# Kernel tuning notes

Hardware: AMD Instinct MI355X
Metric: run time of the kernel (lower is better)

Reference implementation:

```python
import jax, jax.numpy as jnp
import numpy as np

B, S, D, H = 2, 2048, 1024, 16
HEAD_DIM = D // H
WINDOW = 256
DILATION = 1
NEG = jnp.float32(-1e9)


def _build_attn_mask(seq_len):
    # Faithful port of torch _build_attn_mask for causal=True, stencil kind='local'.
    idx = jnp.arange(seq_len)
    diff = idx[None, :] - idx[:, None]  # diff[i, j] = j - i (torch diff is idx.unsqueeze(0)-idx.unsqueeze(1))
    # causal: -inf strictly above diagonal (j > i)
    mask = jnp.where(diff > 0, -jnp.inf, 0.0).astype(jnp.float32)
    # stencil allow: |diff| <= window and |diff| % dilation == 0
    cond = (jnp.abs(diff) <= WINDOW) & (jnp.abs(diff) % DILATION == 0)
    allowed = jnp.where(cond, 0.0, -jnp.inf).astype(jnp.float32)
    # torch.maximum: allow() can UNMASK causally-masked positions inside the window
    mask = jnp.maximum(mask, allowed)
    # clamp(min=-1e9)
    return jnp.maximum(mask, NEG)


def setup_inputs() -> dict:
    key = jax.random.key(0)
    k = jax.random.split(key, 5)
    return {
        "x": jax.random.normal(k[0], (B, S, D), dtype=jnp.float32),
        "in_proj_w": jax.random.normal(k[1], (3 * D, D), dtype=jnp.float32) * (D ** -0.5),
        "in_proj_b": jax.random.normal(k[2], (3 * D,), dtype=jnp.float32) * 0.02,
        "out_proj_w": jax.random.normal(k[3], (D, D), dtype=jnp.float32) * (D ** -0.5),
        "out_proj_b": jax.random.normal(k[4], (D,), dtype=jnp.float32) * 0.02,
    }


def reference(x, in_proj_w, in_proj_b, out_proj_w, out_proj_b):
    b, s, d = x.shape
    # fused qkv projection (torch nn.MultiheadAttention in_proj)
    qkv = x @ in_proj_w.T + in_proj_b  # [b, s, 3d]
    q, k, v = jnp.split(qkv, 3, axis=-1)

    def to_heads(t):
        return t.reshape(b, s, H, HEAD_DIM).transpose(0, 2, 1, 3)  # [b, h, s, hd]

    q, k, v = to_heads(q), to_heads(k), to_heads(v)
    scale = jnp.float32(HEAD_DIM) ** -0.5
    scores = jnp.einsum("bhqd,bhkd->bhqk", q * scale, k)  # [b, h, s, s]
    mask = _build_attn_mask(s)  # [s, s]
    scores = scores + mask[None, None, :, :]
    attn = jax.nn.softmax(scores, axis=-1)
    out = jnp.einsum("bhqk,bhkd->bhqd", attn, v)  # [b, h, s, hd]
    out = out.transpose(0, 2, 1, 3).reshape(b, s, d)
    return out @ out_proj_w.T + out_proj_b
```

## Files before the change

kernel.cpp:

```cpp
#include <hip/hip_runtime.h>
#include <cstddef>

#define BATCH   2
#define SEQ     2048
#define DMODEL  1024
#define NH      16
#define HDIM    64
#define WIN     256
#define MTOT    4096

typedef __bf16 bf16;
typedef __attribute__((ext_vector_type(8)))  __bf16 bf16x8;
typedef __attribute__((ext_vector_type(4)))  float  f32x4;
typedef __attribute__((ext_vector_type(16))) float  f32x16;

#define GLOAD_LDS(gp, lp) __builtin_amdgcn_global_load_lds( \
    (const __attribute__((address_space(1))) void*)(gp),    \
    (__attribute__((address_space(3))) void*)(lp), 16, 0, 0)

__device__ __forceinline__ float fast_exp2(float x) {
#if __has_builtin(__builtin_amdgcn_exp2f)
  return __builtin_amdgcn_exp2f(x);
#else
  float r; asm("v_exp_f32 %0, %1" : "=v"(r) : "v"(x)); return r;
#endif
}

__global__ __launch_bounds__(256)
void cvt_all(const float* __restrict__ x, const float* __restrict__ w1,
             const float* __restrict__ w2, bf16* __restrict__ xh,
             bf16* __restrict__ xl, bf16* __restrict__ w1h,
             bf16* __restrict__ w1l, bf16* __restrict__ w2h,
             bf16* __restrict__ w2l) {
  const int bid = blockIdx.x;
  const float* s; bf16 *hp, *lp; int base;
  if (bid < 2048)      { s = x;  hp = xh;  lp = xl;  base = bid * 2048; }
  else if (bid < 3584) { s = w1; hp = w1h; lp = w1l; base = (bid - 2048) * 2048; }
  else                 { s = w2; hp = w2h; lp = w2l; base = (bid - 3584) * 2048; }
  const int i = base + threadIdx.x * 8;
  float4 a = *(const float4*)(s + i);
  float4 c = *(const float4*)(s + i + 4);
  const float f[8] = {a.x, a.y, a.z, a.w, c.x, c.y, c.z, c.w};
  bf16x8 vh, vl;
#pragma unroll
  for (int j = 0; j < 8; ++j) {
    bf16 hh = (bf16)f[j];
    vh[j] = hh;
    vl[j] = (bf16)(f[j] - (float)hh);
  }
  *(bf16x8*)(hp + i) = vh;
  *(bf16x8*)(lp + i) = vl;
}

__global__ __launch_bounds__(256, 4)
void gemm_qkv_fused(const bf16* __restrict__ xh, const bf16* __restrict__ xl,
                    const bf16* __restrict__ w1h, const bf16* __restrict__ w1l,
                    const float* __restrict__ b1,
                    bf16* __restrict__ Qh, bf16* __restrict__ Ql,
                    bf16* __restrict__ Kt, bf16* __restrict__ Vt) {
  __shared__ bf16 sAh[128 * 32];
  __shared__ bf16 sAl[128 * 32];
  __shared__ bf16 sBh[128 * 32];
  __shared__ bf16 sBl[64 * 32];

  const int t = threadIdx.x, w = t >> 6, lane = t & 63;
  const int ln15 = lane & 15, quad = lane >> 4;
  const int drow = lane >> 2;
  const int dkcol = (lane & 3) * 8;
  const int bid = blockIdx.x;

  if (bid < 512) {
    const int bm = (bid >> 4) * 128;
    const int bn = (bid & 15) * 64;

    f32x4 acc[2][4];
#pragma unroll
    for (int i = 0; i < 2; ++i)
#pragma unroll
      for (int j = 0; j < 4; ++j)
#pragma unroll
        for (int r = 0; r < 4; ++r) acc[i][j][r] = 0.f;

    for (int k0 = 0; k0 < DMODEL; k0 += 32) {
      __syncthreads();
#pragma unroll
      for (int half = 0; half < 2; ++half) {
        const int r = w * 32 + half * 16 + drow;
        const size_t goffA = (size_t)(bm + r) * DMODEL + k0 + dkcol;
        const int loff = (w * 32 + half * 16) * 32;
        GLOAD_LDS(xh + goffA, sAh + loff);
        GLOAD_LDS(xl + goffA, sAl + loff);
      }
      {
        const int r = w * 16 + drow;
        const size_t goffB = (size_t)(bn + r) * DMODEL + k0 + dkcol;
        const int loff = (w * 16) * 32;
        GLOAD_LDS(w1h + goffB, sBh + loff);
        GLOAD_LDS(w1l + goffB, sBl + loff);
      }
      __syncthreads();

      bf16x8 afh[2], afl[2], bfh[4], bfl[4];
#pragma unroll
      for (int mt = 0; mt < 2; ++mt) {
        const int off = (w * 32 + mt * 16 + ln15) * 32 + quad * 8;
        afh[mt] = *(const bf16x8*)&sAh[off];
        afl[mt] = *(const bf16x8*)&sAl[off];
      }
#pragma unroll
      for (int nt = 0; nt < 4; ++nt) {
        const int off = (nt * 16 + ln15) * 32 + quad * 8;
        bfh[nt] = *(const bf16x8*)&sBh[off];
        bfl[nt] = *(const bf16x8*)&sBl[off];
      }
#pragma unroll
      for (int mt = 0; mt < 2; ++mt)
#pragma unroll
        for (int nt = 0; nt < 4; ++nt) {
          acc[mt][nt] = __builtin_amdgcn_mfma_f32_16x16x32_bf16(afh[mt], bfh[nt], acc[mt][nt], 0, 0, 0);
          acc[mt][nt] = __builtin_amdgcn_mfma_f32_16x16x32_bf16(afh[mt], bfl[nt], acc[mt][nt], 0, 0, 0);
          acc[mt][nt] = __builtin_amdgcn_mfma_f32_16x16x32_bf16(afl[mt], bfh[nt], acc[mt][nt], 0, 0, 0);
        }
    }

    float bbcol[4];
#pragma unroll
    for (int nt = 0; nt < 4; ++nt) bbcol[nt] = b1[bn + nt * 16 + ln15];

#pragma unroll
    for (int mt = 0; mt < 2; ++mt)
#pragma unroll
      for (int r = 0; r < 4; ++r) {
        const size_t grow = (size_t)(bm + w * 32 + mt * 16 + quad * 4 + r);
#pragma unroll
        for (int nt = 0; nt < 4; ++nt) {
          const int col = bn + nt * 16 + ln15;
          const float v = acc[mt][nt][r] + bbcol[nt];
          const bf16 hh = (bf16)v;
          Qh[grow * 1024 + col] = hh;
          Ql[grow * 1024 + col] = (bf16)(v - (float)hh);
        }
      }
  } else if (bid < 768) {
    const int kid = bid - 512;
    const int bm = (kid >> 3) * 128, bn = 1024 + (kid & 7) * 128;
    const int wrow = (w & 1) * 64, wcol = (w >> 1) * 64;

    f32x4 acc[4][4];
#pragma unroll
    for (int i = 0; i < 4; ++i)
#pragma unroll
      for (int j = 0; j < 4; ++j)
#pragma unroll
        for (int r = 0; r < 4; ++r) acc[i][j][r] = 0.f;

    for (int k0 = 0; k0 < DMODEL; k0 += 32) {
      __syncthreads();
#pragma unroll
      for (int half = 0; half < 2; ++half) {
        const int r = w * 32 + half * 16 + drow;
        const int loff = (w * 32 + half * 16) * 32;
        GLOAD_LDS(xh + (size_t)(bm + r) * DMODEL + k0 + dkcol, sAh + loff);
        GLOAD_LDS(w1h + (size_t)(bn + r) * DMODEL + k0 + dkcol, sBh + loff);
      }
      __syncthreads();

      bf16x8 af[4], bf[4];
#pragma unroll
      for (int mt = 0; mt < 4; ++mt)
        af[mt] = *(const bf16x8*)&sAh[(wrow + mt * 16 + ln15) * 32 + quad * 8];
#pragma unroll
      for (int nt = 0; nt < 4; ++nt)
        bf[nt] = *(const bf16x8*)&sBh[(wcol + nt * 16 + ln15) * 32 + quad * 8];
#pragma unroll
      for (int mt = 0; mt < 4; ++mt)
#pragma unroll
        for (int nt = 0; nt < 4; ++nt)
          acc[mt][nt] = __builtin_amdgcn_mfma_f32_16x16x32_bf16(af[mt], bf[nt], acc[mt][nt], 0, 0, 0);
    }

    float bbcol[4];
#pragma unroll
    for (int nt = 0; nt < 4; ++nt) bbcol[nt] = b1[bn + wcol + nt * 16 + ln15];

#pragma unroll
    for (int mt = 0; mt < 4; ++mt)
#pragma unroll
      for (int r = 0; r < 4; ++r) {
        const size_t grow = (size_t)(bm + wrow + mt * 16 + quad * 4 + r);
        const int btok = (int)(grow >> 11), key = (int)(grow & 2047);
        const int kt = key >> 6, kw = key & 63;
#pragma unroll
        for (int nt = 0; nt < 4; ++nt) {
          const int col = bn + wcol + nt * 16 + ln15;
          const float v = acc[mt][nt][r] + bbcol[nt];
          const int hh2 = (col - 1024) >> 6, d = col & 63;
          const size_t addr = ((size_t)((btok * 16 + hh2) * 32 + kt) << 12)
                            + (((kw >> 5) * 4 + (d >> 4)) << 9)
                            + ((((d >> 3) & 1) << 5) + (kw & 31)) * 8 + (d & 7);
          Kt[addr] = (bf16)v;
        }
      }
  } else {
    const int vid = bid - 768;
    const int bm = (vid >> 5) * 128, bn = (vid & 31) * 128;
    const int wrow = (w & 1) * 64, wcol = (w >> 1) * 64;
    const bf16* Ah = w1h + 2048 * 1024;
    const float* bias = b1 + 2048;

    f32x4 acc[4][4];
#pragma unroll
    for (int i = 0; i < 4; ++i)
#pragma unroll
      for (int j = 0; j < 4; ++j)
#pragma unroll
        for (int r = 0; r < 4; ++r) acc[i][j][r] = 0.f;

    for (int k0 = 0; k0 < DMODEL; k0 += 32) {
      __syncthreads();
#pragma unroll
      for (int half = 0; half < 2; ++half) {
        const int r = w * 32 + half * 16 + drow;
        const int loff = (w * 32 + half * 16) * 32;
        GLOAD_LDS(Ah + (size_t)(bm + r) * DMODEL + k0 + dkcol, sAh + loff);
        GLOAD_LDS(xh + (size_t)(bn + r) * DMODEL + k0 + dkcol, sBh + loff);
      }
      __syncthreads();

      bf16x8 af[4], bf[4];
#pragma unroll
      for (int mt = 0; mt < 4; ++mt)
        af[mt] = *(const bf16x8*)&sAh[(wrow + mt * 16 + ln15) * 32 + quad * 8];
#pragma unroll
      for (int nt = 0; nt < 4; ++nt)
        bf[nt] = *(const bf16x8*)&sBh[(wcol + nt * 16 + ln15) * 32 + quad * 8];
#pragma unroll
      for (int mt = 0; mt < 4; ++mt)
#pragma unroll
        for (int nt = 0; nt < 4; ++nt)
          acc[mt][nt] = __builtin_amdgcn_mfma_f32_16x16x32_bf16(af[mt], bf[nt], acc[mt][nt], 0, 0, 0);
    }

#pragma unroll
    for (int mt = 0; mt < 4; ++mt)
#pragma unroll
      for (int r = 0; r < 4; ++r) {
        const size_t grow = (size_t)(bm + wrow + mt * 16 + quad * 4 + r);
        const float brow = bias[grow];
        const int hh2 = (int)(grow >> 6), d = (int)(grow & 63);
#pragma unroll
        for (int nt = 0; nt < 4; ++nt) {
          const int col = bn + wcol + nt * 16 + ln15;
          const float v = acc[mt][nt][r] + brow;
          const int btok = col >> 11, key = col & 2047;
          const int kt = key >> 6, kw = key & 63;
          const size_t addr = ((size_t)((btok * 16 + hh2) * 32 + kt) << 12)
                            + (((d >> 5) * 4 + (kw >> 4)) << 9)
                            + ((((kw >> 3) & 1) << 5) + (d & 31)) * 8 + (kw & 7);
          Vt[addr] = (bf16)v;
        }
      }
  }
}

__global__ __launch_bounds__(256)
void gemm_out64(const bf16* __restrict__ Ah, const bf16* __restrict__ Al,
                const bf16* __restrict__ Bh, const bf16* __restrict__ Bl,
                const float* __restrict__ bias, float* __restrict__ Cf) {
  __shared__ bf16 sAh[64 * 32];
  __shared__ bf16 sAl[64 * 32];
  __shared__ bf16 sBh[64 * 32];
  __shared__ bf16 sBl[64 * 32];

  const int t = threadIdx.x, w = t >> 6, lane = t & 63;
  const int ln15 = lane & 15, quad = lane >> 4;
  const int bm = blockIdx.y * 64, bn = blockIdx.x * 64;
  const int wrow = (w & 1) * 32, wcol = (w >> 1) * 32;
  const int drow = lane >> 2;
  const int dkcol = (lane & 3) * 8;

  f32x4 acc[2][2];
#pragma unroll
  for (int i = 0; i < 2; ++i)
#pragma unroll
    for (int j = 0; j < 2; ++j)
#pragma unroll
      for (int r = 0; r < 4; ++r) acc[i][j][r] = 0.f;

  for (int k0 = 0; k0 < DMODEL; k0 += 32) {
    __syncthreads();
    {
      const int r = w * 16 + drow;
      const size_t goffA = (size_t)(bm + r) * DMODEL + k0 + dkcol;
      const size_t goffB = (size_t)(bn + r) * DMODEL + k0 + dkcol;
      const int loff = (w * 16) * 32;
      GLOAD_LDS(Ah + goffA, sAh + loff);
      GLOAD_LDS(Al + goffA, sAl + loff);
      GLOAD_LDS(Bh + goffB, sBh + loff);
      GLOAD_LDS(Bl + goffB, sBl + loff);
    }
    __syncthreads();

    bf16x8 afh[2], afl[2], bfh[2], bfl[2];
#pragma unroll
    for (int mt = 0; mt < 2; ++mt) {
      const int off = (wrow + mt * 16 + ln15) * 32 + quad * 8;
      afh[mt] = *(const bf16x8*)&sAh[off];
      afl[mt] = *(const bf16x8*)&sAl[off];
    }
#pragma unroll
    for (int nt = 0; nt < 2; ++nt) {
      const int off = (wcol + nt * 16 + ln15) * 32 + quad * 8;
      bfh[nt] = *(const bf16x8*)&sBh[off];
      bfl[nt] = *(const bf16x8*)&sBl[off];
    }
#pragma unroll
    for (int mt = 0; mt < 2; ++mt)
#pragma unroll
      for (int nt = 0; nt < 2; ++nt) {
        acc[mt][nt] = __builtin_amdgcn_mfma_f32_16x16x32_bf16(afh[mt], bfh[nt], acc[mt][nt], 0, 0, 0);
        acc[mt][nt] = __builtin_amdgcn_mfma_f32_16x16x32_bf16(afh[mt], bfl[nt], acc[mt][nt], 0, 0, 0);
        acc[mt][nt] = __builtin_amdgcn_mfma_f32_16x16x32_bf16(afl[mt], bfh[nt], acc[mt][nt], 0, 0, 0);
      }
  }

  float bbcol[2];
#pragma unroll
  for (int nt = 0; nt < 2; ++nt) bbcol[nt] = bias[bn + wcol + nt * 16 + ln15];

#pragma unroll
  for (int mt = 0; mt < 2; ++mt)
#pragma unroll
    for (int r = 0; r < 4; ++r) {
      const size_t grow = (size_t)(bm + wrow + mt * 16 + quad * 4 + r);
#pragma unroll
      for (int nt = 0; nt < 2; ++nt) {
        const int col = bn + wcol + nt * 16 + ln15;
        Cf[grow * 1024 + col] = acc[mt][nt][r] + bbcol[nt];
      }
    }
}

__global__ __launch_bounds__(64, 2)
void attn_mfma(const bf16* __restrict__ Qh, const bf16* __restrict__ Ql,
               const bf16* __restrict__ Kt, const bf16* __restrict__ Vt,
               bf16* __restrict__ Omh, bf16* __restrict__ Oml) {
  const int lane = threadIdx.x & 63;
  const int ln31 = lane & 31, half = lane >> 5;
  const int bid = blockIdx.x;
  const int j = bid & 31;
  const int bh = ((j & 7) << 2) | (j >> 3);
  const int c  = 63 - (bid >> 5);
  const int b = bh >> 4, h = bh & 15;
  const int i0w = c * 32;
  const int lim = i0w + WIN;

  __shared__ bf16 sP[32 * 72];

  bf16x8 qh[4], ql[4];
  {
    const size_t rowQ = (size_t)(b * SEQ + i0w + ln31);
#pragma unroll
    for (int ks = 0; ks < 4; ++ks) {
      bf16x8 vh = *(const bf16x8*)(Qh + rowQ * 1024 + h * 64 + ks * 16 + half * 8);
      bf16x8 vl = *(const bf16x8*)(Ql + rowQ * 1024 + h * 64 + ks * 16 + half * 8);
#pragma unroll
      for (int jj = 0; jj < 8; ++jj) {
        float f = ((float)vh[jj] + (float)vl[jj]) * 0.1803368801111204f;
        bf16 hh = (bf16)f;
        qh[ks][jj] = hh;
        ql[ks][jj] = (bf16)(f - (float)hh);
      }
    }
  }
  bf16x8 onesf;
#pragma unroll
  for (int jj = 0; jj < 8; ++jj) onesf[jj] = (ln31 == 0) ? (bf16)1.0f : (bf16)0.0f;

  f32x16 accO0, accO1, accL;
#pragma unroll
  for (int r = 0; r < 16; ++r) { accO0[r] = 0.f; accO1[r] = 0.f; accL[r] = 0.f; }

  const bf16* KtBH = Kt + ((size_t)(b * 16 + h) << 17);
  const bf16* VtBH = Vt + ((size_t)(b * 16 + h) << 17);
  const int lane8 = lane * 8;

  const int nkt = min((i0w + 31 + WIN) / 64 + 1, SEQ / 64);

  for (int kt = 0; kt < nkt; ++kt) {
    const bf16* Kb = KtBH + ((size_t)kt << 12);
    const bf16* Vb = VtBH + ((size_t)kt << 12);

    bf16x8 kf[8], vf[8];
#pragma unroll
    for (int s = 0; s < 8; ++s) {
      kf[s] = *(const bf16x8*)&Kb[(s << 9) + lane8];
      vf[s] = *(const bf16x8*)&Vb[(s << 9) + lane8];
    }

    f32x16 S0, S1;
#pragma unroll
    for (int r = 0; r < 16; ++r) { S0[r] = 0.f; S1[r] = 0.f; }
#pragma unroll
    for (int ks = 0; ks < 4; ++ks) {
      S0 = __builtin_amdgcn_mfma_f32_32x32x16_bf16(qh[ks], kf[ks], S0, 0, 0, 0);
      S0 = __builtin_amdgcn_mfma_f32_32x32x16_bf16(ql[ks], kf[ks], S0, 0, 0, 0);
      S1 = __builtin_amdgcn_mfma_f32_32x32x16_bf16(qh[ks], kf[4 + ks], S1, 0, 0, 0);
      S1 = __builtin_amdgcn_mfma_f32_32x32x16_bf16(ql[ks], kf[4 + ks], S1, 0, 0, 0);
    }

    const int j0 = kt * 64;
#pragma unroll
    for (int cc = 0; cc < 2; ++cc) {
      f32x16& S = cc ? S1 : S0;
      const int vj = j0 + cc * 32 + ln31 - lim;
      const bool may = (j0 + cc * 32 + 31) > lim;
#pragma unroll
      for (int r = 0; r < 16; ++r) {
        const int rl = (r & 3) + 8 * (r >> 2) + 4 * half;
        float pv = fast_exp2(S[r]);
        if (may && (vj > rl)) pv = 0.f;
        sP[rl * 72 + cc * 32 + ln31] = (bf16)pv;
      }
    }

#pragma unroll
    for (int ks = 0; ks < 4; ++ks) {
      bf16x8 pA = *(const bf16x8*)&sP[ln31 * 72 + ks * 16 + half * 8];
      accO0 = __builtin_amdgcn_mfma_f32_32x32x16_bf16(pA, vf[ks], accO0, 0, 0, 0);
      accO1 = __builtin_amdgcn_mfma_f32_32x32x16_bf16(pA, vf[4 + ks], accO1, 0, 0, 0);
      accL  = __builtin_amdgcn_mfma_f32_32x32x16_bf16(pA, onesf, accL, 0, 0, 0);
    }
  }

#pragma unroll
  for (int r = 0; r < 16; ++r) {
    const int rl = (r & 3) + 8 * (r >> 2) + 4 * half;
    const float lv = __shfl(accL[r], lane & 32, 64);
    const float inv = 1.0f / lv;
    const size_t grow = (size_t)(b * SEQ + i0w + rl);
    const int col0 = h * 64 + ln31;
    const float v0 = accO0[r] * inv;
    const float v1 = accO1[r] * inv;
    const bf16 h0 = (bf16)v0, h1 = (bf16)v1;
    Omh[grow * DMODEL + col0]      = h0;
    Oml[grow * DMODEL + col0]      = (bf16)(v0 - (float)h0);
    Omh[grow * DMODEL + col0 + 32] = h1;
    Oml[grow * DMODEL + col0 + 32] = (bf16)(v1 - (float)h1);
  }
}

extern "C" void kernel_launch(void* const* d_in, const int* in_sizes, int n_in,
                              void* d_out, int out_size, void* d_ws, size_t ws_size,
                              hipStream_t stream) {
  const float* x  = (const float*)d_in[0];
  const float* w1 = (const float*)d_in[1];
  const float* b1 = (const float*)d_in[2];
  const float* w2 = (const float*)d_in[3];
  const float* b2 = (const float*)d_in[4];
  float* out = (float*)d_out;

  char* ws = (char*)d_ws;
  bf16* Qh   = (bf16*)(ws + 0);
  bf16* Ql   = (bf16*)(ws + 8388608);
  bf16* Kt   = (bf16*)(ws + 16777216);
  bf16* Vt   = (bf16*)(ws + 25165824);
  bf16* xh   = (bf16*)(ws + 33554432);
  bf16* xl   = (bf16*)(ws + 41943040);
  bf16* w1h  = (bf16*)(ws + 50331648);
  bf16* w1l  = (bf16*)(ws + 56623104);
  bf16* w2h  = (bf16*)(ws + 62914560);
  bf16* w2l  = (bf16*)(ws + 65011712);
  bf16* Omh  = xh;
  bf16* Oml  = xl;

  cvt_all<<<dim3(4096), 256, 0, stream>>>(x, w1, w2, xh, xl, w1h, w1l, w2h, w2l);

  gemm_qkv_fused<<<dim3(1024), 256, 0, stream>>>(
      xh, xl, w1h, w1l, b1, Qh, Ql, Kt, Vt);

  attn_mfma<<<dim3(2048), 64, 0, stream>>>(Qh, Ql, Kt, Vt, Omh, Oml);

  gemm_out64<<<dim3(16, 64), 256, 0, stream>>>(
      Omh, Oml, w2h, w2l, b2, out);
}
```

Before: 239.5 us.

## Split attention KV tiles across two waves with LDS reduction

The attention kernel now runs two wavefronts per block. Each wave handles alternating 64-key tiles with its own LDS P buffer, so the serial KV loop per block is about half as long. The partial O and row-sum accumulators are then combined through LDS, and wave 0 writes the output. This adds several barriers, an LDS round trip, and higher register/LDS pressure per block (launch bounds changed to 128 threads, 4 blocks) in exchange for more parallelism per query tile.

```diff
diff --git a/kernel.cpp b/kernel.cpp
--- a/kernel.cpp
+++ b/kernel.cpp
@@ -341,11 +341,13 @@
     }
 }
 
-__global__ __launch_bounds__(64, 2)
+__global__ __launch_bounds__(128, 4)
 void attn_mfma(const bf16* __restrict__ Qh, const bf16* __restrict__ Ql,
                const bf16* __restrict__ Kt, const bf16* __restrict__ Vt,
                bf16* __restrict__ Omh, bf16* __restrict__ Oml) {
-  const int lane = threadIdx.x & 63;
+  const int t = threadIdx.x;
+  const int wv = t >> 6;
+  const int lane = t & 63;
   const int ln31 = lane & 31, half = lane >> 5;
   const int bid = blockIdx.x;
   const int j = bid & 31;
@@ -355,7 +357,8 @@
   const int i0w = c * 32;
   const int lim = i0w + WIN;
 
-  __shared__ bf16 sP[32 * 72];
+  __shared__ bf16 sPbuf[2][32 * 72];
+  bf16* sP = sPbuf[wv];
 
   bf16x8 qh[4], ql[4];
   {
@@ -387,7 +390,7 @@
 
   const int nkt = min((i0w + 31 + WIN) / 64 + 1, SEQ / 64);
 
-  for (int kt = 0; kt < nkt; ++kt) {
+  for (int kt = wv; kt < nkt; kt += 2) {
     const bf16* Kb = KtBH + ((size_t)kt << 12);
     const bf16* Vb = VtBH + ((size_t)kt << 12);
 
@@ -433,20 +436,48 @@
     }
   }
 
-#pragma unroll
-  for (int r = 0; r < 16; ++r) {
-    const int rl = (r & 3) + 8 * (r >> 2) + 4 * half;
-    const float lv = __shfl(accL[r], lane & 32, 64);
-    const float inv = 1.0f / lv;
-    const size_t grow = (size_t)(b * SEQ + i0w + rl);
-    const int col0 = h * 64 + ln31;
-    const float v0 = accO0[r] * inv;
-    const float v1 = accO1[r] * inv;
-    const bf16 h0 = (bf16)v0, h1 = (bf16)v1;
-    Omh[grow * DMODEL + col0]      = h0;
-    Oml[grow * DMODEL + col0]      = (bf16)(v0 - (float)h0);
-    Omh[grow * DMODEL + col0 + 32] = h1;
-    Oml[grow * DMODEL + col0 + 32] = (bf16)(v1 - (float)h1);
+  float* red = (float*)&sPbuf[0][0];
+  __syncthreads();
+  if (wv == 1) {
+#pragma unroll
+    for (int r = 0; r < 16; ++r) {
+      red[lane * 16 + r]        = accO0[r];
+      red[1024 + lane * 16 + r] = accO1[r];
+    }
+  }
+  __syncthreads();
+  if (wv == 0) {
+#pragma unroll
+    for (int r = 0; r < 16; ++r) {
+      accO0[r] += red[lane * 16 + r];
+      accO1[r] += red[1024 + lane * 16 + r];
+    }
+  }
+  __syncthreads();
+  if (wv == 1) {
+#pragma unroll
+    for (int r = 0; r < 16; ++r) red[lane * 16 + r] = accL[r];
+  }
+  __syncthreads();
+
+  if (wv == 0) {
+#pragma unroll
+    for (int r = 0; r < 16; ++r) accL[r] += red[lane * 16 + r];
+#pragma unroll
+    for (int r = 0; r < 16; ++r) {
+      const int rl = (r & 3) + 8 * (r >> 2) + 4 * half;
+      const float lv = __shfl(accL[r], lane & 32, 64);
+      const float inv = 1.0f / lv;
+      const size_t grow = (size_t)(b * SEQ + i0w + rl);
+      const int col0 = h * 64 + ln31;
+      const float v0 = accO0[r] * inv;
+      const float v1 = accO1[r] * inv;
+      const bf16 h0 = (bf16)v0, h1 = (bf16)v1;
+      Omh[grow * DMODEL + col0]      = h0;
+      Oml[grow * DMODEL + col0]      = (bf16)(v0 - (float)h0);
+      Omh[grow * DMODEL + col0 + 32] = h1;
+      Oml[grow * DMODEL + col0 + 32] = (bf16)(v1 - (float)h1);
+    }
   }
 }
 
@@ -479,7 +510,7 @@
   gemm_qkv_fused<<<dim3(1024), 256, 0, stream>>>(
       xh, xl, w1h, w1l, b1, Qh, Ql, Kt, Vt);
 
-  attn_mfma<<<dim3(2048), 64, 0, stream>>>(Qh, Ql, Kt, Vt, Omh, Oml);
+  attn_mfma<<<dim3(2048), 128, 0, stream>>>(Qh, Ql, Kt, Vt, Omh, Oml);
 
   gemm_out64<<<dim3(16, 64), 256, 0, stream>>>(
       Omh, Oml, w2h, w2l, b2, out);
```

Result: slower. 278.7 us (+16.4%).

## Keep attention probabilities in registers via transposed S and permlane swaps

Applied to the files above, without the earlier changes.

Computes the score tile transposed (K as the A operand) so each lane holds one query column. The exp'd probabilities are then packed to bf16 and redistributed with permlane32_swap directly into the PV MFMA operand layout, which removes the shared-memory round trip for P. It also replaces the ones-vector MFMA row-sum with a per-lane scalar accumulation plus a cross-half shuffle, and raises wave priority around the MFMA blocks. This cuts LDS traffic and one third of the PV MFMAs, at the cost of extra packing and permute instructions and more subtle lane mapping.

```diff
diff --git a/kernel.cpp b/kernel.cpp
--- a/kernel.cpp
+++ b/kernel.cpp
@@ -24,6 +24,12 @@
 #else
   float r; asm("v_exp_f32 %0, %1" : "=v"(r) : "v"(x)); return r;
 #endif
+}
+
+__device__ __forceinline__ unsigned int cvtpk_bf16(float lo, float hi) {
+  unsigned int r;
+  asm("v_cvt_pk_bf16_f32 %0, %1, %2" : "=v"(r) : "v"(lo), "v"(hi));
+  return r;
 }
 
 __global__ __launch_bounds__(256)
@@ -355,8 +361,6 @@
   const int i0w = c * 32;
   const int lim = i0w + WIN;
 
-  __shared__ bf16 sP[32 * 72];
-
   bf16x8 qh[4], ql[4];
   {
     const size_t rowQ = (size_t)(b * SEQ + i0w + ln31);
@@ -373,13 +377,11 @@
       }
     }
   }
-  bf16x8 onesf;
-#pragma unroll
-  for (int jj = 0; jj < 8; ++jj) onesf[jj] = (ln31 == 0) ? (bf16)1.0f : (bf16)0.0f;
-
-  f32x16 accO0, accO1, accL;
-#pragma unroll
-  for (int r = 0; r < 16; ++r) { accO0[r] = 0.f; accO1[r] = 0.f; accL[r] = 0.f; }
+
+  f32x16 accO0, accO1;
+#pragma unroll
+  for (int r = 0; r < 16; ++r) { accO0[r] = 0.f; accO1[r] = 0.f; }
+  float lsum = 0.f;
 
   const bf16* KtBH = Kt + ((size_t)(b * 16 + h) << 17);
   const bf16* VtBH = Vt + ((size_t)(b * 16 + h) << 17);
@@ -401,42 +403,64 @@
     f32x16 S0, S1;
 #pragma unroll
     for (int r = 0; r < 16; ++r) { S0[r] = 0.f; S1[r] = 0.f; }
+    __builtin_amdgcn_s_setprio(1);
 #pragma unroll
     for (int ks = 0; ks < 4; ++ks) {
-      S0 = __builtin_amdgcn_mfma_f32_32x32x16_bf16(qh[ks], kf[ks], S0, 0, 0, 0);
-      S0 = __builtin_amdgcn_mfma_f32_32x32x16_bf16(ql[ks], kf[ks], S0, 0, 0, 0);
-      S1 = __builtin_amdgcn_mfma_f32_32x32x16_bf16(qh[ks], kf[4 + ks], S1, 0, 0, 0);
-      S1 = __builtin_amdgcn_mfma_f32_32x32x16_bf16(ql[ks], kf[4 + ks], S1, 0, 0, 0);
-    }
+      S0 = __builtin_amdgcn_mfma_f32_32x32x16_bf16(kf[ks], qh[ks], S0, 0, 0, 0);
+      S0 = __builtin_amdgcn_mfma_f32_32x32x16_bf16(kf[ks], ql[ks], S0, 0, 0, 0);
+      S1 = __builtin_amdgcn_mfma_f32_32x32x16_bf16(kf[4 + ks], qh[ks], S1, 0, 0, 0);
+      S1 = __builtin_amdgcn_mfma_f32_32x32x16_bf16(kf[4 + ks], ql[ks], S1, 0, 0, 0);
+    }
+    __builtin_amdgcn_s_setprio(0);
 
     const int j0 = kt * 64;
+    bf16x8 pa[4];
 #pragma unroll
     for (int cc = 0; cc < 2; ++cc) {
       f32x16& S = cc ? S1 : S0;
-      const int vj = j0 + cc * 32 + ln31 - lim;
-      const bool may = (j0 + cc * 32 + 31) > lim;
+      const int base = j0 + cc * 32 - lim;
+      const bool may = (base + 31 > 0);
 #pragma unroll
       for (int r = 0; r < 16; ++r) {
-        const int rl = (r & 3) + 8 * (r >> 2) + 4 * half;
+        const int kr = (r & 3) + 8 * (r >> 2) + 4 * half;
         float pv = fast_exp2(S[r]);
-        if (may && (vj > rl)) pv = 0.f;
-        sP[rl * 72 + cc * 32 + ln31] = (bf16)pv;
-      }
-    }
-
+        if (may && (kr + base > ln31)) pv = 0.f;
+        S[r] = pv;
+        lsum += pv;
+      }
+      unsigned int W0[4], W1[4];
+#pragma unroll
+      for (int g = 0; g < 4; ++g) {
+        W0[g] = cvtpk_bf16(S[4 * g + 0], S[4 * g + 1]);
+        W1[g] = cvtpk_bf16(S[4 * g + 2], S[4 * g + 3]);
+      }
+#pragma unroll
+      for (int f = 0; f < 2; ++f) {
+        auto s0 = __builtin_amdgcn_permlane32_swap(W0[2 * f], W0[2 * f + 1], false, false);
+        auto s1 = __builtin_amdgcn_permlane32_swap(W1[2 * f], W1[2 * f + 1], false, false);
+        union { unsigned int w[4]; bf16x8 v; } u;
+        u.w[0] = (unsigned int)s0[0];
+        u.w[1] = (unsigned int)s1[0];
+        u.w[2] = (unsigned int)s0[1];
+        u.w[3] = (unsigned int)s1[1];
+        pa[cc * 2 + f] = u.v;
+      }
+    }
+
+    __builtin_amdgcn_s_setprio(1);
 #pragma unroll
     for (int ks = 0; ks < 4; ++ks) {
-      bf16x8 pA = *(const bf16x8*)&sP[ln31 * 72 + ks * 16 + half * 8];
-      accO0 = __builtin_amdgcn_mfma_f32_32x32x16_bf16(pA, vf[ks], accO0, 0, 0, 0);
-      accO1 = __builtin_amdgcn_mfma_f32_32x32x16_bf16(pA, vf[4 + ks], accO1, 0, 0, 0);
-      accL  = __builtin_amdgcn_mfma_f32_32x32x16_bf16(pA, onesf, accL, 0, 0, 0);
-    }
+      accO0 = __builtin_amdgcn_mfma_f32_32x32x16_bf16(pa[ks], vf[ks], accO0, 0, 0, 0);
+      accO1 = __builtin_amdgcn_mfma_f32_32x32x16_bf16(pa[ks], vf[4 + ks], accO1, 0, 0, 0);
+    }
+    __builtin_amdgcn_s_setprio(0);
   }
 
+  lsum += __shfl_xor(lsum, 32, 64);
 #pragma unroll
   for (int r = 0; r < 16; ++r) {
     const int rl = (r & 3) + 8 * (r >> 2) + 4 * half;
-    const float lv = __shfl(accL[r], lane & 32, 64);
+    const float lv = __shfl(lsum, rl, 64);
     const float inv = 1.0f / lv;
     const size_t grow = (size_t)(b * SEQ + i0w + rl);
     const int col0 = h * 64 + ln31;
```

New measurement: 227.5 us. 5.0% less time.
